# Kernel optimization log

Hardware: AMD Instinct MI355X
Metric: run time of the kernel (lower is better)

Reference implementation:

```python
import jax, jax.numpy as jnp
import numpy as np
import math

HIDDEN = 256
NUM_GAUSSIANS = 64
NUM_FILTERS = 256
CUTOFF = 1.0
COSINE_OFFSET = 0.0
N_NODES = 10000
N_EDGES = 320000


def ssp(x):
    # shifted softplus: softplus(x) - log(2)
    return jax.nn.softplus(x) - jnp.log(2.0).astype(x.dtype)


def setup_inputs() -> dict:
    key = jax.random.key(0)
    ks = jax.random.split(key, 12)

    def xavier(k, fan_out, fan_in):
        a = math.sqrt(6.0 / (fan_in + fan_out))
        return jax.random.uniform(k, (fan_out, fan_in), jnp.float32, -a, a)

    x = jax.random.normal(ks[0], (N_NODES, HIDDEN), jnp.float32)
    ji_pairs = jax.random.randint(ks[1], (2, N_EDGES), 0, N_NODES, jnp.int64)
    e_ji = jax.random.uniform(ks[2], (N_EDGES,), jnp.float32)  # distances in [0, cutoff)
    e_ji_basis = jax.random.normal(ks[3], (N_EDGES, NUM_GAUSSIANS), jnp.float32)

    return {
        "x": x,
        "ji_pairs": ji_pairs,
        "e_ji": e_ji,
        "e_ji_basis": e_ji_basis,
        # filter_nn: Linear(G->F), ssp, Linear(F->F)
        "fw1": xavier(ks[4], NUM_FILTERS, NUM_GAUSSIANS),
        "fb1": jnp.zeros((NUM_FILTERS,), jnp.float32),
        "fw2": xavier(ks[5], NUM_FILTERS, NUM_FILTERS),
        "fb2": jnp.zeros((NUM_FILTERS,), jnp.float32),
        # CFConv linears
        "w1": xavier(ks[6], NUM_FILTERS, HIDDEN),            # linear1, no bias
        "w2": xavier(ks[7], HIDDEN, NUM_FILTERS),            # linear2
        "b2": jnp.zeros((HIDDEN,), jnp.float32),
        # linear3
        "w3": xavier(ks[8], HIDDEN, HIDDEN),
        "b3": jnp.zeros((HIDDEN,), jnp.float32),
    }


def reference(x, ji_pairs, e_ji, e_ji_basis, fw1, fb1, fw2, fb2, w1, w2, b2, w3, b3):
    pi = jnp.asarray(math.pi, x.dtype)
    # cosine cutoff: C = 0.25 * (cos((e - off) * pi / (cutoff - off)) + 1)
    C = 0.25 * (jnp.cos((e_ji - COSINE_OFFSET) * pi / (CUTOFF - COSINE_OFFSET)) + 1.0)
    # filter network on edge RBF features: [E, F]
    W = ssp(e_ji_basis @ fw1.T + fb1) @ fw2.T + fb2
    W = W * C[:, None]
    # linear1 (no bias): [N, F]
    h = x @ w1.T
    # message: x_j * W, gathered from source nodes ji_pairs[0]
    src, dst = ji_pairs[0], ji_pairs[1]
    msg = h[src] * W                                   # [E, F]
    agg = jax.ops.segment_sum(msg, dst, num_segments=x.shape[0])  # [N, F]
    # linear2
    out = agg @ w2.T + b2
    # interaction block tail: act + linear3
    out = ssp(out) @ w3.T + b3
    return out
```

## Files before the change

kernel.cpp:

```cpp
#include <hip/hip_runtime.h>
#include <hip/hip_bf16.h>

typedef __bf16 bf16_t;
typedef float f32x4 __attribute__((ext_vector_type(4)));
typedef __bf16 bf16x8 __attribute__((ext_vector_type(8)));

#define NNODES 10000
#define NEDGES 320000
#define NPAD   10048
#define NB2    (NEDGES / 64)
#define GSLOT  5

#define OFF_AGG   256
#define OFF_JIN   (OFF_AGG  + (size_t)NPAD * 256 * 4)
#define OFF_HIST  (OFF_JIN  + (size_t)2 * NEDGES * 4)
#define OFF_CUR   (OFF_HIST + 10240 * 4)
#define OFF_CSR   (OFF_CUR  + 10240 * 4)
#define OFF_PERM  (OFF_CSR  + 10240 * 4)
#define OFF_SRCS  (OFF_PERM + (size_t)NEDGES * 4)
#define OFF_DSTS  (OFF_SRCS + (size_t)NEDGES * 4)
#define OFF_CES   (OFF_DSTS + (size_t)NEDGES * 4)
#define OFF_CE    (OFF_CES  + (size_t)NEDGES * 4)
#define OFF_WB    (OFF_CE   + (size_t)NEDGES * 4)
#define FW1B 0
#define FW2B 16384
#define W1B  81920
#define W2B  147456
#define W3B  212992
#define FB1B 278528
#define FB2B 278784
#define B2B  279040
#define B3B  279296
#define WBN  279552
#define WS_NEED (OFF_WB + (size_t)WBN * 2)
#define OFF_BASC  ((WS_NEED + 255) & ~(size_t)255)
#define WS_NEED_BIG (OFF_BASC + (size_t)NEDGES * 64 * 2)

__device__ __forceinline__ float ssp_f(float v) {
    return fmaxf(v, 0.f) + __logf(1.f + __expf(-fabsf(v))) - 0.69314718055994531f;
}
__device__ __forceinline__ f32x4 mfma16(bf16x8 a, bf16x8 b, f32x4 c) {
    return __builtin_amdgcn_mfma_f32_16x16x32_bf16(a, b, c, 0, 0, 0);
}
template<bool ISB>
__device__ __forceinline__ bf16x8 ld8(const void* p, size_t off) {
    if constexpr (ISB) return *(const bf16x8*)((const bf16_t*)p + off);
    else {
        const float* f = (const float*)p + off;
        f32x4 lo = *(const f32x4*)f, hi = *(const f32x4*)(f + 4);
        bf16x8 r;
        for (int j = 0; j < 4; ++j) { r[j] = (bf16_t)lo[j]; r[j + 4] = (bf16_t)hi[j]; }
        return r;
    }
}
__device__ __forceinline__ bf16x8 ld8r(bool isb, const void* p, size_t off) {
    if (isb) return *(const bf16x8*)((const bf16_t*)p + off);
    const float* f = (const float*)p + off;
    f32x4 lo = *(const f32x4*)f, hi = *(const f32x4*)(f + 4);
    bf16x8 r;
    for (int j = 0; j < 4; ++j) { r[j] = (bf16_t)lo[j]; r[j + 4] = (bf16_t)hi[j]; }
    return r;
}
template<bool ISB>
__device__ __forceinline__ void st1(void* p, size_t off, float v) {
    if constexpr (ISB) ((bf16_t*)p)[off] = (bf16_t)v;
    else               ((float*)p)[off] = v;
}
__device__ __forceinline__ float ld1r(bool isb, const void* p, size_t off) {
    return isb ? (float)((const bf16_t*)p)[off] : ((const float*)p)[off];
}

__global__ __launch_bounds__(256) void detect_kernel(
    const void* __restrict__ x, const int* __restrict__ jraw,
    int* __restrict__ flags, int* __restrict__ hist)
{
    __shared__ int cnt, hi;
    if (threadIdx.x == 0) { cnt = 0; hi = 0; }
    __syncthreads();
    const unsigned short* xw = (const unsigned short*)x;
    int local = 0;
    for (int i = threadIdx.x; i < 2048; i += 256) {
        unsigned int e = (xw[2 * i] >> 7) & 0xFF;
        if (e >= 100 && e <= 141) local++;
    }
    atomicAdd(&cnt, local);
    int v = 0;
    for (int i = threadIdx.x; i < 1024; i += 256) v |= jraw[2 * i + 1];
    if (v != 0) atomicOr(&hi, 1);
    for (int i = threadIdx.x; i < 10240; i += 256) hist[i] = 0;
    __syncthreads();
    if (threadIdx.x == 0) { flags[0] = (cnt > 1024) ? 1 : 0; flags[1] = (hi == 0) ? 1 : 0; }
}

__global__ __launch_bounds__(256) void prep_kernel(
    const int* __restrict__ raw, const int* __restrict__ flags,
    const void* __restrict__ e_ji, const void* __restrict__ basis,
    const void* fw1, const void* fb1, const void* fw2, const void* fb2,
    const void* w1, const void* w2, const void* b2, const void* w3, const void* b3,
    int* __restrict__ jin, int* __restrict__ hist, float* __restrict__ ce,
    bf16_t* __restrict__ wb, float* __restrict__ agg,
    bf16_t* __restrict__ basc0, int doconv)
{
    const bool is64 = (flags[1] != 0);
    const bool isb  = (flags[0] != 0);
    const int gid = blockIdx.x * 256 + threadIdx.x;
    if (gid < 2 * NEDGES) {
        int iv = is64 ? raw[2 * gid] : raw[gid];
        iv = iv < 0 ? 0 : (iv >= NNODES ? NNODES - 1 : iv);
        jin[gid] = iv;
        if (gid >= NEDGES) atomicAdd(&hist[iv], 1);
    }
    if (gid < NEDGES)
        ce[gid] = 0.25f * (cosf(3.14159265358979f * ld1r(isb, e_ji, gid)) + 1.0f);
    if (gid < WBN) {
        int g = gid; const void* s; int so;
        if      (g < FW2B) { s = fw1; so = g - FW1B; }
        else if (g < W1B)  { s = fw2; so = g - FW2B; }
        else if (g < W2B)  { s = w1;  so = g - W1B; }
        else if (g < W3B)  { s = w2;  so = g - W2B; }
        else if (g < FB1B) { s = w3;  so = g - W3B; }
        else if (g < FB2B) { s = fb1; so = g - FB1B; }
        else if (g < B2B)  { s = fb2; so = g - FB2B; }
        else if (g < B3B)  { s = b2;  so = g - B2B; }
        else               { s = b3;  so = g - B3B; }
        wb[gid] = (bf16_t)ld1r(isb, s, so);
    }
    f32x4 z = {0.f, 0.f, 0.f, 0.f};
    for (int i = gid; i < NPAD * 256 / 4; i += 2500 * 256)
        ((f32x4*)agg)[i] = z;
    if (doconv) {
        const int nv = NEDGES * 64 / 8;
        for (int i = gid; i < nv; i += 2500 * 256)
            ((bf16x8*)basc0)[i] = ld8r(isb, basis, (size_t)i * 8);
    }
}

__global__ __launch_bounds__(256) void scan_kernel(
    const int* __restrict__ hist, int* __restrict__ cur, int* __restrict__ csr)
{
    __shared__ int s[256];
    const int t = threadIdx.x;
    int loc[40]; int sum = 0;
    const int base = t * 40;
    for (int j = 0; j < 40; ++j) {
        int i = base + j;
        loc[j] = (i < NNODES) ? hist[i] : 0;
        sum += loc[j];
    }
    s[t] = sum; __syncthreads();
    for (int off = 1; off < 256; off <<= 1) {
        int v = (t >= off) ? s[t - off] : 0;
        __syncthreads();
        if (t >= off) s[t] += v;
        __syncthreads();
    }
    int pre = (t == 0) ? 0 : s[t - 1];
    for (int j = 0; j < 40; ++j) {
        int i = base + j;
        cur[i] = pre;
        csr[i] = pre;
        pre += loc[j];
    }
}

__global__ __launch_bounds__(256) void scatter_kernel(
    const int* __restrict__ jin, const float* __restrict__ ce,
    int* __restrict__ cur, int* __restrict__ perm,
    int* __restrict__ src_s, int* __restrict__ dst_s, float* __restrict__ ce_s)
{
    int e = blockIdx.x * 256 + threadIdx.x;
    if (e < NEDGES) {
        int d = jin[NEDGES + e];
        int pos = atomicAdd(&cur[d], 1);
        perm[pos]  = e;
        src_s[pos] = jin[e];
        dst_s[pos] = d;
        ce_s[pos]  = ce[e];
    }
}

template<bool ISB>
__global__ __launch_bounds__(256, 2) void h_gemm_kernel(
    const void* __restrict__ x, const bf16_t* __restrict__ wb,
    bf16_t* __restrict__ h, const int* __restrict__ flags)
{
    if ((flags[0] != 0) != ISB) return;
    const bf16_t* w1b = wb + W1B;
    const int w = threadIdx.x >> 6, L = threadIdx.x & 63;
    const int lane16 = L & 15, quad = L >> 4;
    const int nb = blockIdx.x * 64, cb = w * 64;
    f32x4 acc[4][4] = {};
    for (int kc = 0; kc < 8; ++kc) {
        const int ko = kc * 32 + quad * 8;
        bf16x8 af[4], bfr[4];
        for (int mt = 0; mt < 4; ++mt) {
            int row = nb + mt * 16 + lane16;
            if (row >= NNODES) row = NNODES - 1;
            af[mt] = ld8<ISB>(x, (size_t)row * 256 + ko);
        }
        for (int nt = 0; nt < 4; ++nt)
            bfr[nt] = *(const bf16x8*)(w1b + (size_t)(cb + nt * 16 + lane16) * 256 + ko);
        for (int mt = 0; mt < 4; ++mt)
            for (int nt = 0; nt < 4; ++nt)
                acc[mt][nt] = mfma16(af[mt], bfr[nt], acc[mt][nt]);
    }
    for (int mt = 0; mt < 4; ++mt)
        for (int r = 0; r < 4; ++r) {
            int row = nb + mt * 16 + quad * 4 + r;
            if (row < NNODES)
                for (int nt = 0; nt < 4; ++nt)
                    h[(size_t)row * 256 + cb + nt * 16 + lane16] = (bf16_t)acc[mt][nt][r];
        }
}

__global__ __launch_bounds__(256, 4) void edge_half_kernel(
    const bf16_t* __restrict__ basc0, const int* __restrict__ perm,
    const int* __restrict__ src_s, const int* __restrict__ dst_s,
    const float* __restrict__ ce_s,
    const bf16_t* __restrict__ wb, const bf16_t* __restrict__ h,
    float* __restrict__ agg)
{
    __shared__ bf16_t T[64][264];
    __shared__ float G[GSLOT][132];
    __shared__ int sperm[64], ssrc[64], sdst[64];
    __shared__ float sce[64];
    const int tid = threadIdx.x;
    const int w = tid >> 6, L = tid & 63;
    const int lane16 = L & 15, quad = L >> 4;
    const int bid  = (int)blockIdx.x;
    const int xcd8 = bid & 7;
    const int hf   = xcd8 >> 2;
    const int tile = (xcd8 & 3) * 1250 + (bid >> 3);
    const int e0   = tile * 64;
    const int cb1  = w * 64;
    const int mh   = w >> 1, cg = w & 1;
    const int cb2  = hf * 128 + cg * 64;

    if      (w == 0) sperm[L] = perm[e0 + L];
    else if (w == 1) ssrc[L] = src_s[e0 + L];
    else if (w == 2) sdst[L] = dst_s[e0 + L];
    else             sce[L]  = ce_s[e0 + L];
    for (int i = tid; i < GSLOT * 132; i += 256) (&G[0][0])[i] = 0.f;

    const bf16_t* fw1b = wb + FW1B;
    const bf16_t* fw2b = wb + FW2B;
    float fb1v[4], fb2v[4];
    for (int nt = 0; nt < 4; ++nt) {
        fb1v[nt] = (float)wb[FB1B + cb1 + nt * 16 + lane16];
        fb2v[nt] = (float)wb[FB2B + cb2 + nt * 16 + lane16];
    }
    __syncthreads();

    const int sbase = sdst[0];
    const int span  = sdst[63] - sbase + 1;
    const bool fbk  = (span > GSLOT);

    const int hrow = tid >> 2, hseg = tid & 3;
    bf16x8 hreg[4];
    {
        const bf16_t* hs = h + (size_t)ssrc[hrow] * 256 + hf * 128 + hseg * 32;
        #pragma unroll
        for (int j = 0; j < 4; ++j) hreg[j] = ((const bf16x8*)hs)[j];
    }

    int prow[4];
    for (int mt = 0; mt < 4; ++mt) prow[mt] = sperm[mt * 16 + lane16];

    f32x4 acc1[4][4] = {};
    for (int kc = 0; kc < 2; ++kc) {
        const int ko = kc * 32 + quad * 8;
        bf16x8 af[4], bfr[4];
        for (int mt = 0; mt < 4; ++mt)
            af[mt] = *(const bf16x8*)(basc0 + (size_t)prow[mt] * 64 + ko);
        for (int nt = 0; nt < 4; ++nt)
            bfr[nt] = *(const bf16x8*)(fw1b + (size_t)(cb1 + nt * 16 + lane16) * 64 + ko);
        for (int mt = 0; mt < 4; ++mt)
            for (int nt = 0; nt < 4; ++nt)
                acc1[mt][nt] = mfma16(af[mt], bfr[nt], acc1[mt][nt]);
    }
    for (int nt = 0; nt < 4; ++nt) {
        int col = cb1 + nt * 16 + lane16;
        for (int mt = 0; mt < 4; ++mt)
            for (int r = 0; r < 4; ++r)
                T[mt * 16 + quad * 4 + r][col] = (bf16_t)ssp_f(acc1[mt][nt][r] + fb1v[nt]);
    }
    __syncthreads();

    f32x4 acc2[2][4] = {};
    for (int kc = 0; kc < 8; ++kc) {
        const int ko = kc * 32 + quad * 8;
        bf16x8 af[2], bfr[4];
        for (int mt = 0; mt < 2; ++mt)
            af[mt] = *(const bf16x8*)(&T[mh * 32 + mt * 16 + lane16][ko]);
        for (int nt = 0; nt < 4; ++nt)
            bfr[nt] = *(const bf16x8*)(fw2b + (size_t)(cb2 + nt * 16 + lane16) * 256 + ko);
        for (int mt = 0; mt < 2; ++mt)
            for (int nt = 0; nt < 4; ++nt)
                acc2[mt][nt] = mfma16(af[mt], bfr[nt], acc2[mt][nt]);
    }
    __syncthreads();

    {
        bf16_t* dp = &T[hrow][hseg * 32];
        #pragma unroll
        for (int j = 0; j < 4; ++j) ((bf16x8*)dp)[j] = hreg[j];
    }
    __syncthreads();

    float run[4] = {0, 0, 0, 0};
    int curn = -1;
    for (int mt = 0; mt < 2; ++mt)
        for (int r = 0; r < 4; ++r) {
            int row = mh * 32 + mt * 16 + quad * 4 + r;
            int n = sdst[row];
            if (n != curn) {
                if (curn >= 0) {
                    if (!fbk)
                        for (int nt = 0; nt < 4; ++nt)
                            atomicAdd(&G[curn - sbase][cg * 64 + nt * 16 + lane16], run[nt]);
                    else
                        for (int nt = 0; nt < 4; ++nt)
                            atomicAdd(&agg[(size_t)curn * 256 + cb2 + nt * 16 + lane16], run[nt]);
                }
                curn = n;
                run[0] = run[1] = run[2] = run[3] = 0.f;
            }
            float cv = sce[row];
            for (int nt = 0; nt < 4; ++nt)
                run[nt] += (acc2[mt][nt][r] + fb2v[nt]) * cv *
                           (float)T[row][cg * 64 + nt * 16 + lane16];
        }
    if (curn >= 0) {
        if (!fbk)
            for (int nt = 0; nt < 4; ++nt)
                atomicAdd(&G[curn - sbase][cg * 64 + nt * 16 + lane16], run[nt]);
        else
            for (int nt = 0; nt < 4; ++nt)
                atomicAdd(&agg[(size_t)curn * 256 + cb2 + nt * 16 + lane16], run[nt]);
    }
    __syncthreads();

    if (!fbk && tid < 128) {
        for (int s = 0; s < span; ++s)
            atomicAdd(&agg[(size_t)(sbase + s) * 256 + hf * 128 + tid], G[s][tid]);
    }
}

template<bool ISB>
__global__ __launch_bounds__(256, 4) void edge_kernel_sp(
    const void* __restrict__ basis, const int* __restrict__ perm,
    const int* __restrict__ src_s, const int* __restrict__ dst_s,
    const float* __restrict__ ce_s,
    const bf16_t* __restrict__ wb, const bf16_t* __restrict__ h,
    float* __restrict__ agg, const int* __restrict__ flags)
{
    if ((flags[0] != 0) != ISB) return;
    __shared__ bf16_t T[64][264];
    __shared__ float G[GSLOT][260];
    __shared__ int sperm[64], ssrc[64], sdst[64];
    __shared__ float sce[64];
    const int tid = threadIdx.x;
    const int w = tid >> 6, L = tid & 63;
    const int lane16 = L & 15, quad = L >> 4;
    const int cb = w * 64;
    const int bid = (int)blockIdx.x;
    const int e0 = ((bid & 7) * (NB2 / 8) + (bid >> 3)) * 64;

    if      (w == 0) sperm[L] = perm[e0 + L];
    else if (w == 1) ssrc[L] = src_s[e0 + L];
    else if (w == 2) sdst[L] = dst_s[e0 + L];
    else             sce[L]  = ce_s[e0 + L];
    for (int i = tid; i < GSLOT * 260; i += 256) (&G[0][0])[i] = 0.f;

    const bf16_t* fw1b = wb + FW1B;
    const bf16_t* fw2b = wb + FW2B;
    float fb1v[4], fb2v[4];
    for (int nt = 0; nt < 4; ++nt) {
        fb1v[nt] = (float)wb[FB1B + cb + nt * 16 + lane16];
        fb2v[nt] = (float)wb[FB2B + cb + nt * 16 + lane16];
    }
    __syncthreads();

    const int sbase = sdst[0];
    const int span  = sdst[63] - sbase + 1;
    const bool fbk  = (span > GSLOT);

    const int hrow = tid >> 2, hseg = tid & 3;
    bf16x8 hreg[8];
    {
        const bf16_t* hs = h + (size_t)ssrc[hrow] * 256 + hseg * 64;
        #pragma unroll
        for (int j = 0; j < 8; ++j) hreg[j] = ((const bf16x8*)hs)[j];
    }

    int prow[4];
    for (int mt = 0; mt < 4; ++mt) prow[mt] = sperm[mt * 16 + lane16];

    f32x4 acc1[4][4] = {};
    for (int kc = 0; kc < 2; ++kc) {
        const int ko = kc * 32 + quad * 8;
        bf16x8 af[4], bfr[4];
        for (int mt = 0; mt < 4; ++mt)
            af[mt] = ld8<ISB>(basis, (size_t)prow[mt] * 64 + ko);
        for (int nt = 0; nt < 4; ++nt)
            bfr[nt] = *(const bf16x8*)(fw1b + (size_t)(cb + nt * 16 + lane16) * 64 + ko);
        for (int mt = 0; mt < 4; ++mt)
            for (int nt = 0; nt < 4; ++nt)
                acc1[mt][nt] = mfma16(af[mt], bfr[nt], acc1[mt][nt]);
    }
    for (int nt = 0; nt < 4; ++nt) {
        int col = cb + nt * 16 + lane16;
        for (int mt = 0; mt < 4; ++mt)
            for (int r = 0; r < 4; ++r)
                T[mt * 16 + quad * 4 + r][col] = (bf16_t)ssp_f(acc1[mt][nt][r] + fb1v[nt]);
    }
    __syncthreads();

    f32x4 acc2[4][4] = {};
    for (int kc = 0; kc < 8; ++kc) {
        const int ko = kc * 32 + quad * 8;
        bf16x8 af[4], bfr[4];
        for (int mt = 0; mt < 4; ++mt)
            af[mt] = *(const bf16x8*)(&T[mt * 16 + lane16][ko]);
        for (int nt = 0; nt < 4; ++nt)
            bfr[nt] = *(const bf16x8*)(fw2b + (size_t)(cb + nt * 16 + lane16) * 256 + ko);
        for (int mt = 0; mt < 4; ++mt)
            for (int nt = 0; nt < 4; ++nt)
                acc2[mt][nt] = mfma16(af[mt], bfr[nt], acc2[mt][nt]);
    }
    __syncthreads();

    {
        bf16_t* dp = &T[hrow][hseg * 64];
        #pragma unroll
        for (int j = 0; j < 8; ++j) ((bf16x8*)dp)[j] = hreg[j];
    }
    __syncthreads();

    float run[4] = {0, 0, 0, 0};
    int curn = -1;
    for (int mt = 0; mt < 4; ++mt)
        for (int r = 0; r < 4; ++r) {
            int row = mt * 16 + quad * 4 + r;
            int n = sdst[row];
            if (n != curn) {
                if (curn >= 0) {
                    if (!fbk)
                        for (int nt = 0; nt < 4; ++nt)
                            atomicAdd(&G[curn - sbase][cb + nt * 16 + lane16], run[nt]);
                    else
                        for (int nt = 0; nt < 4; ++nt)
                            atomicAdd(&agg[(size_t)curn * 256 + cb + nt * 16 + lane16], run[nt]);
                }
                curn = n;
                run[0] = run[1] = run[2] = run[3] = 0.f;
            }
            float cv = sce[row];
            for (int nt = 0; nt < 4; ++nt) {
                int col = cb + nt * 16 + lane16;
                run[nt] += (acc2[mt][nt][r] + fb2v[nt]) * cv * (float)T[row][col];
            }
        }
    if (curn >= 0) {
        if (!fbk)
            for (int nt = 0; nt < 4; ++nt)
                atomicAdd(&G[curn - sbase][cb + nt * 16 + lane16], run[nt]);
        else
            for (int nt = 0; nt < 4; ++nt)
                atomicAdd(&agg[(size_t)curn * 256 + cb + nt * 16 + lane16], run[nt]);
    }
    __syncthreads();

    if (!fbk) {
        for (int s = 0; s < span; ++s)
            atomicAdd(&agg[(size_t)(sbase + s) * 256 + tid], G[s][tid]);
    }
}

template<bool ISB>
__global__ __launch_bounds__(256, 2) void out_kernel(
    const float* __restrict__ agg, const bf16_t* __restrict__ wb,
    void* __restrict__ out, const int* __restrict__ flags)
{
    if ((flags[0] != 0) != ISB) return;
    const bf16_t* w2b = wb + W2B;
    const bf16_t* w3b = wb + W3B;
    __shared__ bf16_t U[64][264];
    const int w = threadIdx.x >> 6, L = threadIdx.x & 63;
    const int lane16 = L & 15, quad = L >> 4;
    const int nb = blockIdx.x * 64, cb = w * 64;

    f32x4 acc[4][4] = {};
    for (int kc = 0; kc < 8; ++kc) {
        const int ko = kc * 32 + quad * 8;
        bf16x8 af[4], bfr[4];
        for (int mt = 0; mt < 4; ++mt) {
            int row = nb + mt * 16 + lane16;
            const float* p = agg + (size_t)row * 256 + ko;
            f32x4 lo = *(const f32x4*)p, hi = *(const f32x4*)(p + 4);
            bf16x8 a;
            for (int j = 0; j < 4; ++j) { a[j] = (bf16_t)lo[j]; a[j + 4] = (bf16_t)hi[j]; }
            af[mt] = a;
        }
        for (int nt = 0; nt < 4; ++nt)
            bfr[nt] = *(const bf16x8*)(w2b + (size_t)(cb + nt * 16 + lane16) * 256 + ko);
        for (int mt = 0; mt < 4; ++mt)
            for (int nt = 0; nt < 4; ++nt)
                acc[mt][nt] = mfma16(af[mt], bfr[nt], acc[mt][nt]);
    }
    for (int nt = 0; nt < 4; ++nt) {
        int col = cb + nt * 16 + lane16;
        float bias = (float)wb[B2B + col];
        for (int mt = 0; mt < 4; ++mt)
            for (int r = 0; r < 4; ++r)
                U[mt * 16 + quad * 4 + r][col] = (bf16_t)ssp_f(acc[mt][nt][r] + bias);
    }
    __syncthreads();

    f32x4 acc2[4][4] = {};
    for (int kc = 0; kc < 8; ++kc) {
        const int ko = kc * 32 + quad * 8;
        bf16x8 af[4], bfr[4];
        for (int mt = 0; mt < 4; ++mt)
            af[mt] = *(const bf16x8*)(&U[mt * 16 + lane16][ko]);
        for (int nt = 0; nt < 4; ++nt)
            bfr[nt] = *(const bf16x8*)(w3b + (size_t)(cb + nt * 16 + lane16) * 256 + ko);
        for (int mt = 0; mt < 4; ++mt)
            for (int nt = 0; nt < 4; ++nt)
                acc2[mt][nt] = mfma16(af[mt], bfr[nt], acc2[mt][nt]);
    }
    for (int mt = 0; mt < 4; ++mt)
        for (int r = 0; r < 4; ++r) {
            int row = nb + mt * 16 + quad * 4 + r;
            if (row < NNODES)
                for (int nt = 0; nt < 4; ++nt) {
                    int col = cb + nt * 16 + lane16;
                    st1<ISB>(out, (size_t)row * 256 + col,
                             acc2[mt][nt][r] + (float)wb[B3B + col]);
                }
        }
}

extern "C" void kernel_launch(void* const* d_in, const int* in_sizes, int n_in,
                              void* d_out, int out_size, void* d_ws, size_t ws_size,
                              hipStream_t stream) {
    const void* x     = d_in[0];
    const int*  ji    = (const int*)d_in[1];
    const void* e_ji  = d_in[2];
    const void* basis = d_in[3];
    const void* fw1   = d_in[4];
    const void* fb1   = d_in[5];
    const void* fw2   = d_in[6];
    const void* fb2   = d_in[7];
    const void* w1    = d_in[8];
    const void* w2    = d_in[9];
    const void* b2    = d_in[10];
    const void* w3    = d_in[11];
    const void* b3    = d_in[12];

    if (ws_size < WS_NEED) return;
    const bool bigws = ws_size >= WS_NEED_BIG;

    char* W = (char*)d_ws;
    int*    flags = (int*)W;
    float*  agg   = (float*)(W + OFF_AGG);
    int*    jin   = (int*)(W + OFF_JIN);
    int*    hist  = (int*)(W + OFF_HIST);
    int*    cur   = (int*)(W + OFF_CUR);
    int*    csr   = (int*)(W + OFF_CSR);
    int*    perm  = (int*)(W + OFF_PERM);
    int*    src_s = (int*)(W + OFF_SRCS);
    int*    dst_s = (int*)(W + OFF_DSTS);
    float*  ce_s  = (float*)(W + OFF_CES);
    float*  ce    = (float*)(W + OFF_CE);
    bf16_t* wb    = (bf16_t*)(W + OFF_WB);
    bf16_t* basc0 = (bf16_t*)(W + OFF_BASC);
    bf16_t* h     = (bf16_t*)d_out;

    detect_kernel<<<1, 256, 0, stream>>>(x, ji, flags, hist);
    prep_kernel<<<2500, 256, 0, stream>>>(ji, flags, e_ji, basis, fw1, fb1, fw2, fb2,
                                          w1, w2, b2, w3, b3, jin, hist, ce, wb, agg,
                                          basc0, bigws ? 1 : 0);
    scan_kernel<<<1, 256, 0, stream>>>(hist, cur, csr);
    scatter_kernel<<<1250, 256, 0, stream>>>(jin, ce, cur, perm, src_s, dst_s, ce_s);
    h_gemm_kernel<true ><<<157, 256, 0, stream>>>(x, wb, h, flags);
    h_gemm_kernel<false><<<157, 256, 0, stream>>>(x, wb, h, flags);
    if (bigws) {
        edge_half_kernel<<<2 * NB2, 256, 0, stream>>>(basc0, perm, src_s, dst_s, ce_s, wb, h, agg);
    } else {
        edge_kernel_sp<true ><<<NB2, 256, 0, stream>>>(basis, perm, src_s, dst_s, ce_s, wb, h, agg, flags);
        edge_kernel_sp<false><<<NB2, 256, 0, stream>>>(basis, perm, src_s, dst_s, ce_s, wb, h, agg, flags);
    }
    out_kernel<true ><<<157, 256, 0, stream>>>(agg, wb, d_out, flags);
    out_kernel<false><<<157, 256, 0, stream>>>(agg, wb, d_out, flags);
}
```

Measured before the change: 532.6 us.

## Split edge filter GEMM across K halves into quarter blocks and merge dual-variant launches

The edge kernel now launches four blocks per 64-edge tile instead of two. Each block computes only half of the first filter layer's hidden columns and the matching K-half partial of the second filter GEMM, then scatter-adds its partial message, which is valid because the message is linear in W. The bias is added only by the kh=0 half. This halves LDS and register use per block so occupancy can rise to 7 blocks, at the cost of doubling the gathered h and basis loads and the atomic adds into agg. Separately, the paired bf16/f32 template launches for the h GEMM and output kernels are merged into single launches that branch on the flag at runtime.

```diff
diff --git a/kernel.cpp b/kernel.cpp
--- a/kernel.cpp
+++ b/kernel.cpp
@@ -180,11 +180,10 @@
 }
 
 template<bool ISB>
-__global__ __launch_bounds__(256, 2) void h_gemm_kernel(
+__device__ __forceinline__ void h_gemm_body(
     const void* __restrict__ x, const bf16_t* __restrict__ wb,
-    bf16_t* __restrict__ h, const int* __restrict__ flags)
-{
-    if ((flags[0] != 0) != ISB) return;
+    bf16_t* __restrict__ h)
+{
     const bf16_t* w1b = wb + W1B;
     const int w = threadIdx.x >> 6, L = threadIdx.x & 63;
     const int lane16 = L & 15, quad = L >> 4;
@@ -212,15 +211,22 @@
                     h[(size_t)row * 256 + cb + nt * 16 + lane16] = (bf16_t)acc[mt][nt][r];
         }
 }
-
-__global__ __launch_bounds__(256, 4) void edge_half_kernel(
+__global__ __launch_bounds__(256, 2) void h_gemm_kernel(
+    const void* __restrict__ x, const bf16_t* __restrict__ wb,
+    bf16_t* __restrict__ h, const int* __restrict__ flags)
+{
+    if (flags[0] != 0) h_gemm_body<true >(x, wb, h);
+    else               h_gemm_body<false>(x, wb, h);
+}
+
+__global__ __launch_bounds__(256, 7) void edge_quarter_kernel(
     const bf16_t* __restrict__ basc0, const int* __restrict__ perm,
     const int* __restrict__ src_s, const int* __restrict__ dst_s,
     const float* __restrict__ ce_s,
     const bf16_t* __restrict__ wb, const bf16_t* __restrict__ h,
     float* __restrict__ agg)
 {
-    __shared__ bf16_t T[64][264];
+    __shared__ bf16_t T[64][136];
     __shared__ float G[GSLOT][132];
     __shared__ int sperm[64], ssrc[64], sdst[64];
     __shared__ float sce[64];
@@ -230,11 +236,12 @@
     const int bid  = (int)blockIdx.x;
     const int xcd8 = bid & 7;
     const int hf   = xcd8 >> 2;
-    const int tile = (xcd8 & 3) * 1250 + (bid >> 3);
+    const int chunk = xcd8 & 3;
+    const int r8   = bid >> 3;
+    const int kh   = r8 & 1;
+    const int tile = chunk * 1250 + (r8 >> 1);
     const int e0   = tile * 64;
-    const int cb1  = w * 64;
-    const int mh   = w >> 1, cg = w & 1;
-    const int cb2  = hf * 128 + cg * 64;
+    const int cw0  = w * 32;
 
     if      (w == 0) sperm[L] = perm[e0 + L];
     else if (w == 1) ssrc[L] = src_s[e0 + L];
@@ -244,10 +251,10 @@
 
     const bf16_t* fw1b = wb + FW1B;
     const bf16_t* fw2b = wb + FW2B;
-    float fb1v[4], fb2v[4];
-    for (int nt = 0; nt < 4; ++nt) {
-        fb1v[nt] = (float)wb[FB1B + cb1 + nt * 16 + lane16];
-        fb2v[nt] = (float)wb[FB2B + cb2 + nt * 16 + lane16];
+    float fb1v[2], fb2v[2];
+    for (int nt = 0; nt < 2; ++nt) {
+        fb1v[nt] = (float)wb[FB1B + kh * 128 + cw0 + nt * 16 + lane16];
+        fb2v[nt] = kh ? 0.f : (float)wb[FB2B + hf * 128 + cw0 + nt * 16 + lane16];
     }
     __syncthreads();
 
@@ -266,36 +273,38 @@
     int prow[4];
     for (int mt = 0; mt < 4; ++mt) prow[mt] = sperm[mt * 16 + lane16];
 
-    f32x4 acc1[4][4] = {};
+    f32x4 acc1[4][2] = {};
     for (int kc = 0; kc < 2; ++kc) {
         const int ko = kc * 32 + quad * 8;
-        bf16x8 af[4], bfr[4];
+        bf16x8 af[4], bfr[2];
         for (int mt = 0; mt < 4; ++mt)
             af[mt] = *(const bf16x8*)(basc0 + (size_t)prow[mt] * 64 + ko);
-        for (int nt = 0; nt < 4; ++nt)
-            bfr[nt] = *(const bf16x8*)(fw1b + (size_t)(cb1 + nt * 16 + lane16) * 64 + ko);
-        for (int mt = 0; mt < 4; ++mt)
-            for (int nt = 0; nt < 4; ++nt)
+        for (int nt = 0; nt < 2; ++nt)
+            bfr[nt] = *(const bf16x8*)(fw1b +
+                (size_t)(kh * 128 + cw0 + nt * 16 + lane16) * 64 + ko);
+        for (int mt = 0; mt < 4; ++mt)
+            for (int nt = 0; nt < 2; ++nt)
                 acc1[mt][nt] = mfma16(af[mt], bfr[nt], acc1[mt][nt]);
     }
-    for (int nt = 0; nt < 4; ++nt) {
-        int col = cb1 + nt * 16 + lane16;
+    for (int nt = 0; nt < 2; ++nt) {
+        int col = cw0 + nt * 16 + lane16;
         for (int mt = 0; mt < 4; ++mt)
             for (int r = 0; r < 4; ++r)
                 T[mt * 16 + quad * 4 + r][col] = (bf16_t)ssp_f(acc1[mt][nt][r] + fb1v[nt]);
     }
     __syncthreads();
 
-    f32x4 acc2[2][4] = {};
-    for (int kc = 0; kc < 8; ++kc) {
+    f32x4 acc2[4][2] = {};
+    for (int kc = 0; kc < 4; ++kc) {
         const int ko = kc * 32 + quad * 8;
-        bf16x8 af[2], bfr[4];
-        for (int mt = 0; mt < 2; ++mt)
-            af[mt] = *(const bf16x8*)(&T[mh * 32 + mt * 16 + lane16][ko]);
-        for (int nt = 0; nt < 4; ++nt)
-            bfr[nt] = *(const bf16x8*)(fw2b + (size_t)(cb2 + nt * 16 + lane16) * 256 + ko);
-        for (int mt = 0; mt < 2; ++mt)
-            for (int nt = 0; nt < 4; ++nt)
+        bf16x8 af[4], bfr[2];
+        for (int mt = 0; mt < 4; ++mt)
+            af[mt] = *(const bf16x8*)(&T[mt * 16 + lane16][ko]);
+        for (int nt = 0; nt < 2; ++nt)
+            bfr[nt] = *(const bf16x8*)(fw2b +
+                (size_t)(hf * 128 + cw0 + nt * 16 + lane16) * 256 + kh * 128 + ko);
+        for (int mt = 0; mt < 4; ++mt)
+            for (int nt = 0; nt < 2; ++nt)
                 acc2[mt][nt] = mfma16(af[mt], bfr[nt], acc2[mt][nt]);
     }
     __syncthreads();
@@ -307,42 +316,44 @@
     }
     __syncthreads();
 
-    float run[4] = {0, 0, 0, 0};
+    float run[2] = {0, 0};
     int curn = -1;
-    for (int mt = 0; mt < 2; ++mt)
+    for (int mt = 0; mt < 4; ++mt)
         for (int r = 0; r < 4; ++r) {
-            int row = mh * 32 + mt * 16 + quad * 4 + r;
+            int row = mt * 16 + quad * 4 + r;
             int n = sdst[row];
             if (n != curn) {
                 if (curn >= 0) {
                     if (!fbk)
-                        for (int nt = 0; nt < 4; ++nt)
-                            atomicAdd(&G[curn - sbase][cg * 64 + nt * 16 + lane16], run[nt]);
+                        for (int nt = 0; nt < 2; ++nt)
+                            atomicAdd(&G[curn - sbase][cw0 + nt * 16 + lane16], run[nt]);
                     else
-                        for (int nt = 0; nt < 4; ++nt)
-                            atomicAdd(&agg[(size_t)curn * 256 + cb2 + nt * 16 + lane16], run[nt]);
+                        for (int nt = 0; nt < 2; ++nt)
+                            atomicAdd(&agg[(size_t)curn * 256 + hf * 128 + cw0 + nt * 16 + lane16], run[nt]);
                 }
                 curn = n;
-                run[0] = run[1] = run[2] = run[3] = 0.f;
+                run[0] = run[1] = 0.f;
             }
             float cv = sce[row];
-            for (int nt = 0; nt < 4; ++nt)
-                run[nt] += (acc2[mt][nt][r] + fb2v[nt]) * cv *
-                           (float)T[row][cg * 64 + nt * 16 + lane16];
+            for (int nt = 0; nt < 2; ++nt) {
+                int cw = cw0 + nt * 16 + lane16;
+                run[nt] += (acc2[mt][nt][r] + fb2v[nt]) * cv * (float)T[row][cw];
+            }
         }
     if (curn >= 0) {
         if (!fbk)
-            for (int nt = 0; nt < 4; ++nt)
-                atomicAdd(&G[curn - sbase][cg * 64 + nt * 16 + lane16], run[nt]);
+            for (int nt = 0; nt < 2; ++nt)
+                atomicAdd(&G[curn - sbase][cw0 + nt * 16 + lane16], run[nt]);
         else
-            for (int nt = 0; nt < 4; ++nt)
-                atomicAdd(&agg[(size_t)curn * 256 + cb2 + nt * 16 + lane16], run[nt]);
-    }
-    __syncthreads();
-
-    if (!fbk && tid < 128) {
-        for (int s = 0; s < span; ++s)
-            atomicAdd(&agg[(size_t)(sbase + s) * 256 + hf * 128 + tid], G[s][tid]);
+            for (int nt = 0; nt < 2; ++nt)
+                atomicAdd(&agg[(size_t)curn * 256 + hf * 128 + cw0 + nt * 16 + lane16], run[nt]);
+    }
+    __syncthreads();
+
+    if (!fbk) {
+        const int c = tid & 127;
+        for (int s = tid >> 7; s < span; s += 2)
+            atomicAdd(&agg[(size_t)(sbase + s) * 256 + hf * 128 + c], G[s][c]);
     }
 }
 
@@ -478,14 +489,13 @@
 }
 
 template<bool ISB>
-__global__ __launch_bounds__(256, 2) void out_kernel(
+__device__ __forceinline__ void out_body(
     const float* __restrict__ agg, const bf16_t* __restrict__ wb,
-    void* __restrict__ out, const int* __restrict__ flags)
-{
-    if ((flags[0] != 0) != ISB) return;
+    void* __restrict__ out, bf16_t* __restrict__ Ubuf)
+{
     const bf16_t* w2b = wb + W2B;
     const bf16_t* w3b = wb + W3B;
-    __shared__ bf16_t U[64][264];
+    bf16_t (*U)[264] = (bf16_t(*)[264])Ubuf;
     const int w = threadIdx.x >> 6, L = threadIdx.x & 63;
     const int lane16 = L & 15, quad = L >> 4;
     const int nb = blockIdx.x * 64, cb = w * 64;
@@ -539,6 +549,14 @@
                              acc2[mt][nt][r] + (float)wb[B3B + col]);
                 }
         }
+}
+__global__ __launch_bounds__(256, 2) void out_kernel(
+    const float* __restrict__ agg, const bf16_t* __restrict__ wb,
+    void* __restrict__ out, const int* __restrict__ flags)
+{
+    __shared__ bf16_t U[64][264];
+    if (flags[0] != 0) out_body<true >(agg, wb, out, &U[0][0]);
+    else               out_body<false>(agg, wb, out, &U[0][0]);
 }
 
 extern "C" void kernel_launch(void* const* d_in, const int* in_sizes, int n_in,
@@ -583,14 +601,12 @@
                                           basc0, bigws ? 1 : 0);
     scan_kernel<<<1, 256, 0, stream>>>(hist, cur, csr);
     scatter_kernel<<<1250, 256, 0, stream>>>(jin, ce, cur, perm, src_s, dst_s, ce_s);
-    h_gemm_kernel<true ><<<157, 256, 0, stream>>>(x, wb, h, flags);
-    h_gemm_kernel<false><<<157, 256, 0, stream>>>(x, wb, h, flags);
+    h_gemm_kernel<<<157, 256, 0, stream>>>(x, wb, h, flags);
     if (bigws) {
-        edge_half_kernel<<<2 * NB2, 256, 0, stream>>>(basc0, perm, src_s, dst_s, ce_s, wb, h, agg);
+        edge_quarter_kernel<<<4 * NB2, 256, 0, stream>>>(basc0, perm, src_s, dst_s, ce_s, wb, h, agg);
     } else {
         edge_kernel_sp<true ><<<NB2, 256, 0, stream>>>(basis, perm, src_s, dst_s, ce_s, wb, h, agg, flags);
         edge_kernel_sp<false><<<NB2, 256, 0, stream>>>(basis, perm, src_s, dst_s, ce_s, wb, h, agg, flags);
     }
-    out_kernel<true ><<<157, 256, 0, stream>>>(agg, wb, d_out, flags);
-    out_kernel<false><<<157, 256, 0, stream>>>(agg, wb, d_out, flags);
-}
+    out_kernel<<<157, 256, 0, stream>>>(agg, wb, d_out, flags);
+}
```

New measurement: 537.7 us. No clear change (+1.0%).
